# Performance work log

Hardware: AMD Instinct MI355X
Metric: run time of the kernel (lower is better)

The kernel has to match this reference:

```python
import jax, jax.numpy as jnp
import numpy as np

B, S, A, H, E = 8192, 256, 64, 1024, 8
IN = S + A
OUT = S + 1


def setup_inputs() -> dict:
    key = jax.random.key(0)
    ks = jax.random.split(key, 8)
    state = jax.random.normal(ks[0], (B, S), dtype=jnp.float32)
    action = jax.random.normal(ks[1], (B, A), dtype=jnp.float32)
    idx = jax.random.randint(ks[2], (B,), 0, E, dtype=jnp.int32)
    # Kaiming-ish scaling to keep activations sane
    W1 = jax.random.normal(ks[3], (E, IN, H), dtype=jnp.float32) / np.sqrt(IN)
    b1 = jnp.zeros((E, H), dtype=jnp.float32)
    W2 = jax.random.normal(ks[4], (E, H, H), dtype=jnp.float32) / np.sqrt(H)
    b2 = jnp.zeros((E, H), dtype=jnp.float32)
    W3 = jax.random.normal(ks[5], (E, H, OUT), dtype=jnp.float32) / np.sqrt(H)
    b3 = jnp.zeros((E, OUT), dtype=jnp.float32)
    return {"state": state, "action": action, "idx": idx,
            "W1": W1, "b1": b1, "W2": W2, "b2": b2, "W3": W3, "b3": b3}


def reference(state, action, idx, W1, b1, W2, b2, W3, b3):
    # Dense-MoE style: run all E experts on the full batch, then select the
    # per-sample expert output chosen by idx (matches masked gather/scatter
    # in the torch predict loop).
    x = jnp.concatenate([state, action], axis=-1)                  # [B, IN]
    h = jax.nn.relu(jnp.einsum('bi,eih->beh', x, W1) + b1)         # [B, E, H]
    h = jax.nn.relu(jnp.einsum('beh,ehk->bek', h, W2) + b2)        # [B, E, H]
    out = jnp.einsum('beh,eho->beo', h, W3) + b3                   # [B, E, S+1]
    sel = jnp.take_along_axis(out, idx[:, None, None], axis=1)[:, 0]  # [B, S+1]
    s_dim = state.shape[-1]
    delta = sel[:, :s_dim]
    reward = sel[:, s_dim:]
    next_state = state + delta
    return next_state, reward
```

## Files before the change

kernel.cpp:

```cpp
#include <hip/hip_runtime.h>
#include <stdint.h>

#define B_SZ   8192
#define IN_DIM 320
#define H_DIM  1024
#define E_NUM  8
#define OUT_DIM 257
#define TM     64
#define MAXT   (B_SZ / TM + E_NUM)

typedef __bf16 bf16x8 __attribute__((ext_vector_type(8)));
typedef float  f32x4  __attribute__((ext_vector_type(4)));

typedef unsigned int __attribute__((address_space(1))) as1_uint;
typedef unsigned int __attribute__((address_space(3))) as3_uint;

__device__ __forceinline__ void gload_lds16(const void* g, void* l) {
    __builtin_amdgcn_global_load_lds((const as1_uint*)g, (as3_uint*)l, 16, 0, 0);
}

__device__ __forceinline__ unsigned short f2bf(float f) {
    unsigned int u = __float_as_uint(f);
    return (unsigned short)((u + 0x7fffu + ((u >> 16) & 1u)) >> 16);
}

__global__ __launch_bounds__(256)
void k_prep(const float* __restrict__ state, const float* __restrict__ action,
            const int* __restrict__ idx,
            const float* __restrict__ W1, const float* __restrict__ W2,
            const float* __restrict__ W3,
            unsigned short* __restrict__ xb, unsigned short* __restrict__ w1t,
            unsigned short* __restrict__ w2t, unsigned short* __restrict__ w3t,
            int* __restrict__ order, int* __restrict__ te,
            int* __restrict__ tp0, int* __restrict__ tcnt) {
    __shared__ unsigned short tileU[64][65];
    __shared__ int scnt[16][E_NUM];
    int bid = blockIdx.x, tid = threadIdx.x;

    if (bid == 0) {
        int shard = tid & 15;
        if (tid < 128) ((int*)scnt)[tid] = 0;
        __syncthreads();
        for (int b = tid; b < B_SZ; b += 256) atomicAdd(&scnt[shard][idx[b]], 1);
        __syncthreads();
        if (tid == 0) {
            int pos = 0, tt = 0;
            for (int e = 0; e < E_NUM; e++) {
                int start = pos;
                for (int s = 0; s < 16; s++) { int c = scnt[s][e]; scnt[s][e] = pos; pos += c; }
                int tot = pos - start;
                for (int st = 0; st < tot; st += TM) {
                    te[tt] = e; tp0[tt] = start + st; tcnt[tt] = min(TM, tot - st); tt++;
                }
            }
            for (; tt < MAXT; tt++) { te[tt] = 0; tp0[tt] = 0; tcnt[tt] = 0; }
        }
        __syncthreads();
        for (int b = tid; b < B_SZ; b += 256) {
            int e = idx[b];
            int p = atomicAdd(&scnt[shard][e], 1);
            order[p] = b;
        }
        return;
    }

    if (bid <= 2560) {
        int q = (bid - 1) * 256 + tid;
        int b = q / 80, j = q % 80;
        float4 v = (j < 64) ? ((const float4*)state)[b * 64 + j]
                            : ((const float4*)action)[b * 16 + (j - 64)];
        ushort4 o;
        o.x = f2bf(v.x); o.y = f2bf(v.y); o.z = f2bf(v.z); o.w = f2bf(v.w);
        ((ushort4*)xb)[q] = o;
        return;
    }

    if (bid < 5761) {
        int e, kt, nt, K, Nsrc, dstRows; bool vec;
        const float* src; unsigned short* dst;
        if (bid < 3201) {
            int r = bid - 2561; e = r / 80; int m = r % 80; kt = m / 16; nt = m % 16;
            K = IN_DIM; Nsrc = H_DIM; dstRows = H_DIM; src = W1; dst = w1t; vec = true;
        } else if (bid < 5249) {
            int r = bid - 3201; e = r / 256; int m = r % 256; kt = m / 16; nt = m % 16;
            K = H_DIM; Nsrc = H_DIM; dstRows = H_DIM; src = W2; dst = w2t; vec = true;
        } else {
            int r = bid - 5249; e = r / 64; int m = r % 64; kt = m / 4; nt = m % 4;
            K = H_DIM; Nsrc = OUT_DIM; dstRows = 320; src = W3; dst = w3t; vec = false;
        }
        int k0 = kt * 64, n0 = nt * 64;
        const float* s = src + (size_t)e * K * Nsrc;
        unsigned short* d = dst + (size_t)e * dstRows * K;
        int c4 = (tid & 15) * 4;
        int rb = tid >> 4;

#pragma unroll
        for (int p = 0; p < 4; p++) {
            int r = rb + p * 16;
            const float* sp = s + (size_t)(k0 + r) * Nsrc + n0 + c4;
            float4 v;
            if (vec) v = *(const float4*)sp;
            else { v.x = sp[0]; v.y = sp[1]; v.z = sp[2]; v.w = sp[3]; }
            tileU[r][c4 + 0] = f2bf(v.x);
            tileU[r][c4 + 1] = f2bf(v.y);
            tileU[r][c4 + 2] = f2bf(v.z);
            tileU[r][c4 + 3] = f2bf(v.w);
        }
        __syncthreads();
#pragma unroll
        for (int p = 0; p < 4; p++) {
            int n = rb + p * 16;
            ushort4 o;
            o.x = tileU[c4 + 0][n];
            o.y = tileU[c4 + 1][n];
            o.z = tileU[c4 + 2][n];
            o.w = tileU[c4 + 3][n];
            *(ushort4*)&d[(size_t)(n0 + n) * K + k0 + c4] = o;
        }
        return;
    }

    int i = (bid - 5761) * 256 + tid;
    int e = i >> 10, k = i & 1023;
    w3t[((size_t)e * 320 + 256) * H_DIM + k] =
        f2bf(W3[((size_t)e * H_DIM + k) * OUT_DIM + 256]);
}

template <int K, int TN, int WN, bool GATHER, int MODE>
__global__ __launch_bounds__(256, 2)
void k_gemm(const unsigned short* __restrict__ Abase,
            const unsigned short* __restrict__ Wt, int wtRows,
            const float* __restrict__ bias, int bstride,
            unsigned short* __restrict__ Hout,
            float* __restrict__ Out, const float* __restrict__ state,
            const int* __restrict__ order,
            const int* __restrict__ te, const int* __restrict__ tp0,
            const int* __restrict__ tcnt) {
    constexpr int NI  = K / 32;
    constexpr int NF  = WN / 16;
    constexpr int ABY = 64 * 64;
    constexpr int BBY = TN * 64;
    constexpr int STG = ABY + BBY;
    __shared__ __align__(16) char lds[2 * STG];

    int t = blockIdx.x;
    int cnt = tcnt[t];
    if (cnt == 0) return;
    int e = te[t], p0 = tp0[t];
    int n0 = blockIdx.y * TN;
    int tid = threadIdx.x;
    int w = tid >> 6, lane = tid & 63;

    int r  = tid >> 2;
    int cg = (tid & 3) ^ ((r >> 1) & 3);
    int rc = r < cnt ? r : cnt - 1;
    long arow = GATHER ? order[p0 + rc] : (p0 + rc);
    const unsigned short* aP = Abase + (size_t)arow * K + cg * 8;
    const unsigned short* bP = Wt + ((size_t)e * wtRows + n0 + r) * K + cg * 8;

    auto stage = [&](int k0, int sb) {
        gload_lds16(aP + k0, lds + sb + tid * 16);
        gload_lds16(bP + k0, lds + sb + ABY + tid * 16);
        if (TN == 128)
            gload_lds16(bP + (size_t)64 * K + k0, lds + sb + ABY + 4096 + tid * 16);
    };

    f32x4 acc[4][NF];
#pragma unroll
    for (int i = 0; i < 4; i++)
#pragma unroll
        for (int j = 0; j < NF; j++) acc[i][j] = (f32x4)0.f;

    const int fm   = lane & 15;
    const int kc   = lane >> 4;
    const int koff = ((kc ^ ((fm >> 1) & 3)) * 8);

    stage(0, 0);
    for (int it = 0; it < NI; ++it) {
        __syncthreads();
        if (it + 1 < NI) stage((it + 1) * 32, ((it + 1) & 1) * STG);
        const unsigned short* As = (const unsigned short*)(lds + (it & 1) * STG);
        const unsigned short* Bs = As + ABY / 2;

        bf16x8 af[4], bf[NF];
#pragma unroll
        for (int i = 0; i < 4; i++)
            af[i] = *(const bf16x8*)&As[(i * 16 + fm) * 32 + koff];
#pragma unroll
        for (int j = 0; j < NF; j++)
            bf[j] = *(const bf16x8*)&Bs[(w * WN + j * 16 + fm) * 32 + koff];
#pragma unroll
        for (int i = 0; i < 4; i++)
#pragma unroll
            for (int j = 0; j < NF; j++)
                acc[i][j] = __builtin_amdgcn_mfma_f32_16x16x32_bf16(
                    af[i], bf[j], acc[i][j], 0, 0, 0);
    }

    int col = lane & 15, rq = lane >> 4;
#pragma unroll
    for (int j = 0; j < NF; j++) {
        int n = n0 + w * WN + j * 16 + col;
        float bv = (MODE == 0) ? bias[e * bstride + n]
                               : ((n <= 256) ? bias[e * bstride + n] : 0.f);
#pragma unroll
        for (int i = 0; i < 4; i++) {
#pragma unroll
            for (int rr = 0; rr < 4; rr++) {
                int m = i * 16 + rq * 4 + rr;
                if (m < cnt) {
                    float v = acc[i][j][rr] + bv;
                    if (MODE == 0) {
                        Hout[(size_t)(p0 + m) * H_DIM + n] = f2bf(fmaxf(v, 0.f));
                    } else {
                        int row = order[p0 + m];
                        if (n < 256) {
                            size_t o = (size_t)row * 256 + n;
                            Out[o] = state[o] + v;
                        } else if (n == 256) {
                            Out[(size_t)B_SZ * 256 + row] = v;
                        }
                    }
                }
            }
        }
    }
}

extern "C" void kernel_launch(void* const* d_in, const int* in_sizes, int n_in,
                              void* d_out, int out_size, void* d_ws, size_t ws_size,
                              hipStream_t stream) {
    const float* state  = (const float*)d_in[0];
    const float* action = (const float*)d_in[1];
    const int*   idx    = (const int*)d_in[2];
    const float* W1     = (const float*)d_in[3];
    const float* b1     = (const float*)d_in[4];
    const float* W2     = (const float*)d_in[5];
    const float* b2     = (const float*)d_in[6];
    const float* W3     = (const float*)d_in[7];
    const float* b3     = (const float*)d_in[8];
    float* out = (float*)d_out;

    char* ws = (char*)d_ws;
    size_t off = 0;
    auto alloc = [&](size_t bytes) -> void* {
        void* p = ws + off;
        off = (off + bytes + 255) & ~(size_t)255;
        return p;
    };
    unsigned short* xb  = (unsigned short*)alloc((size_t)B_SZ * IN_DIM * 2);
    unsigned short* w1t = (unsigned short*)alloc((size_t)E_NUM * H_DIM * IN_DIM * 2);
    unsigned short* w2t = (unsigned short*)alloc((size_t)E_NUM * H_DIM * H_DIM * 2);
    unsigned short* w3t = (unsigned short*)alloc((size_t)E_NUM * 320 * H_DIM * 2);
    unsigned short* h1  = (unsigned short*)alloc((size_t)B_SZ * H_DIM * 2);
    unsigned short* h2  = (unsigned short*)alloc((size_t)B_SZ * H_DIM * 2);
    int* order = (int*)alloc(B_SZ * 4);
    int* te    = (int*)alloc(MAXT * 4);
    int* tp0   = (int*)alloc(MAXT * 4);
    int* tcnt  = (int*)alloc(MAXT * 4);

    k_prep<<<5793, 256, 0, stream>>>(state, action, idx, W1, W2, W3,
                                     xb, w1t, w2t, w3t, order, te, tp0, tcnt);

    k_gemm<IN_DIM, 128, 32, true, 0><<<dim3(MAXT, 8), 256, 0, stream>>>(
        xb, w1t, H_DIM, b1, H_DIM, h1, nullptr, nullptr, order, te, tp0, tcnt);
    k_gemm<H_DIM, 128, 32, false, 0><<<dim3(MAXT, 8), 256, 0, stream>>>(
        h1, w2t, H_DIM, b2, H_DIM, h2, nullptr, nullptr, order, te, tp0, tcnt);
    k_gemm<H_DIM, 64, 16, false, 1><<<dim3(MAXT, 5), 256, 0, stream>>>(
        h2, w3t, 320, b3, OUT_DIM, nullptr, out, state, order, te, tp0, tcnt);
}
```

Baseline: 225.7 us.

## Enlarge grouped GEMM M-tile to 128 rows with 2x2 wave layout

Doubles the per-block row tile from 64 to 128 tokens and arranges the four waves as a 2x2 grid (two along M, two along N) instead of four waves along N. Each weight tile loaded into LDS is now reused across twice as many rows, which cuts weight traffic and halves the number of row tiles. The cost is more LDS per block, fewer blocks in flight, and more padding waste in the last partial tile of each expert.

Measured after the change: 227.6 us. No clear change (+0.9%).

```diff
diff --git a/kernel.cpp b/kernel.cpp
--- a/kernel.cpp
+++ b/kernel.cpp
@@ -6,7 +6,7 @@
 #define H_DIM  1024
 #define E_NUM  8
 #define OUT_DIM 257
-#define TM     64
+#define TM     128
 #define MAXT   (B_SZ / TM + E_NUM)
 
 typedef __bf16 bf16x8 __attribute__((ext_vector_type(8)));
@@ -126,7 +126,7 @@
         f2bf(W3[((size_t)e * H_DIM + k) * OUT_DIM + 256]);
 }
 
-template <int K, int TN, int WN, bool GATHER, int MODE>
+template <int K, int TN, bool GATHER, int MODE>
 __global__ __launch_bounds__(256, 2)
 void k_gemm(const unsigned short* __restrict__ Abase,
             const unsigned short* __restrict__ Wt, int wtRows,
@@ -137,10 +137,12 @@
             const int* __restrict__ te, const int* __restrict__ tp0,
             const int* __restrict__ tcnt) {
     constexpr int NI  = K / 32;
+    constexpr int WN  = TN / 2;
     constexpr int NF  = WN / 16;
-    constexpr int ABY = 64 * 64;
+    constexpr int ABY = 128 * 64;
     constexpr int BBY = TN * 64;
     constexpr int STG = ABY + BBY;
+    constexpr int BL  = TN / 64;
     __shared__ __align__(16) char lds[2 * STG];
 
     int t = blockIdx.x;
@@ -150,19 +152,25 @@
     int n0 = blockIdx.y * TN;
     int tid = threadIdx.x;
     int w = tid >> 6, lane = tid & 63;
-
-    int r  = tid >> 2;
-    int cg = (tid & 3) ^ ((r >> 1) & 3);
-    int rc = r < cnt ? r : cnt - 1;
-    long arow = GATHER ? order[p0 + rc] : (p0 + rc);
-    const unsigned short* aP = Abase + (size_t)arow * K + cg * 8;
-    const unsigned short* bP = Wt + ((size_t)e * wtRows + n0 + r) * K + cg * 8;
+    int wm = w >> 1, wn = w & 1;
+
+    int r0 = tid >> 2;
+    int cg = (tid & 3) ^ ((r0 >> 1) & 3);
+    int rc0 = r0 < cnt ? r0 : cnt - 1;
+    int rc1 = (r0 + 64) < cnt ? (r0 + 64) : cnt - 1;
+    long a0 = GATHER ? order[p0 + rc0] : (p0 + rc0);
+    long a1 = GATHER ? order[p0 + rc1] : (p0 + rc1);
+    const unsigned short* aP0 = Abase + (size_t)a0 * K + cg * 8;
+    const unsigned short* aP1 = Abase + (size_t)a1 * K + cg * 8;
+    const unsigned short* bP0 = Wt + ((size_t)e * wtRows + n0 + r0) * K + cg * 8;
+    const unsigned short* bP1 = bP0 + (size_t)64 * K;
 
     auto stage = [&](int k0, int sb) {
-        gload_lds16(aP + k0, lds + sb + tid * 16);
-        gload_lds16(bP + k0, lds + sb + ABY + tid * 16);
-        if (TN == 128)
-            gload_lds16(bP + (size_t)64 * K + k0, lds + sb + ABY + 4096 + tid * 16);
+        gload_lds16(aP0 + k0, lds + sb + tid * 16);
+        gload_lds16(aP1 + k0, lds + sb + 4096 + tid * 16);
+        gload_lds16(bP0 + k0, lds + sb + ABY + tid * 16);
+        if (BL == 2)
+            gload_lds16(bP1 + k0, lds + sb + ABY + 4096 + tid * 16);
     };
 
     f32x4 acc[4][NF];
@@ -179,8 +187,9 @@
     for (int it = 0; it < NI; ++it) {
         __syncthreads();
         if (it + 1 < NI) stage((it + 1) * 32, ((it + 1) & 1) * STG);
-        const unsigned short* As = (const unsigned short*)(lds + (it & 1) * STG);
-        const unsigned short* Bs = As + ABY / 2;
+        const unsigned short* Ls = (const unsigned short*)(lds + (it & 1) * STG);
+        const unsigned short* As = Ls + wm * 64 * 32;
+        const unsigned short* Bs = Ls + ABY / 2 + wn * WN * 32;
 
         bf16x8 af[4], bf[NF];
 #pragma unroll
@@ -188,7 +197,7 @@
             af[i] = *(const bf16x8*)&As[(i * 16 + fm) * 32 + koff];
 #pragma unroll
         for (int j = 0; j < NF; j++)
-            bf[j] = *(const bf16x8*)&Bs[(w * WN + j * 16 + fm) * 32 + koff];
+            bf[j] = *(const bf16x8*)&Bs[(j * 16 + fm) * 32 + koff];
 #pragma unroll
         for (int i = 0; i < 4; i++)
 #pragma unroll
@@ -200,14 +209,14 @@
     int col = lane & 15, rq = lane >> 4;
 #pragma unroll
     for (int j = 0; j < NF; j++) {
-        int n = n0 + w * WN + j * 16 + col;
+        int n = n0 + wn * WN + j * 16 + col;
         float bv = (MODE == 0) ? bias[e * bstride + n]
                                : ((n <= 256) ? bias[e * bstride + n] : 0.f);
 #pragma unroll
         for (int i = 0; i < 4; i++) {
 #pragma unroll
             for (int rr = 0; rr < 4; rr++) {
-                int m = i * 16 + rq * 4 + rr;
+                int m = wm * 64 + i * 16 + rq * 4 + rr;
                 if (m < cnt) {
                     float v = acc[i][j][rr] + bv;
                     if (MODE == 0) {
@@ -262,10 +271,10 @@
     k_prep<<<5793, 256, 0, stream>>>(state, action, idx, W1, W2, W3,
                                      xb, w1t, w2t, w3t, order, te, tp0, tcnt);
 
-    k_gemm<IN_DIM, 128, 32, true, 0><<<dim3(MAXT, 8), 256, 0, stream>>>(
+    k_gemm<IN_DIM, 128, true, 0><<<dim3(MAXT, 8), 256, 0, stream>>>(
         xb, w1t, H_DIM, b1, H_DIM, h1, nullptr, nullptr, order, te, tp0, tcnt);
-    k_gemm<H_DIM, 128, 32, false, 0><<<dim3(MAXT, 8), 256, 0, stream>>>(
+    k_gemm<H_DIM, 128, false, 0><<<dim3(MAXT, 8), 256, 0, stream>>>(
         h1, w2t, H_DIM, b2, H_DIM, h2, nullptr, nullptr, order, te, tp0, tcnt);
-    k_gemm<H_DIM, 64, 16, false, 1><<<dim3(MAXT, 5), 256, 0, stream>>>(
+    k_gemm<H_DIM, 64, false, 1><<<dim3(MAXT, 5), 256, 0, stream>>>(
         h2, w3t, 320, b3, OUT_DIM, nullptr, out, state, order, te, tp0, tcnt);
 }
```

## Use 128x128 tiles with a K=64 stage, 2x2 warp layout, and coarser prep blocks

Applied to the files above, without the earlier changes.

Restructures the grouped GEMM so each stage loads a 64-wide K slice with an 8-chunk XOR swizzle. Warps are arranged 2x2 over the output tile, and layers 1-2 switch to 128x128 tiles with their own 128-row tile schedule and a swapped grid order, so blocks sharing an expert tile run close together. The aim is more MFMA work per LDS load and fewer sync points per unit of work. The prep kernel is also coarsened so each block handles several tiles, cutting the block count. Larger tiles mean more padding waste on partial expert groups and fewer blocks to fill the CUs.

Result: slower. 235.1 us (+4.2%).

```diff
diff --git a/kernel.cpp b/kernel.cpp
--- a/kernel.cpp
+++ b/kernel.cpp
@@ -6,8 +6,8 @@
 #define H_DIM  1024
 #define E_NUM  8
 #define OUT_DIM 257
-#define TM     64
-#define MAXT   (B_SZ / TM + E_NUM)
+#define MAXT1  72
+#define MAXT2  136
 
 typedef __bf16 bf16x8 __attribute__((ext_vector_type(8)));
 typedef float  f32x4  __attribute__((ext_vector_type(4)));
@@ -31,8 +31,9 @@
             const float* __restrict__ W3,
             unsigned short* __restrict__ xb, unsigned short* __restrict__ w1t,
             unsigned short* __restrict__ w2t, unsigned short* __restrict__ w3t,
-            int* __restrict__ order, int* __restrict__ te,
-            int* __restrict__ tp0, int* __restrict__ tcnt) {
+            int* __restrict__ order,
+            int* __restrict__ te1, int* __restrict__ tp1, int* __restrict__ tc1,
+            int* __restrict__ te2, int* __restrict__ tp2, int* __restrict__ tc2) {
     __shared__ unsigned short tileU[64][65];
     __shared__ int scnt[16][E_NUM];
     int bid = blockIdx.x, tid = threadIdx.x;
@@ -44,16 +45,20 @@
         for (int b = tid; b < B_SZ; b += 256) atomicAdd(&scnt[shard][idx[b]], 1);
         __syncthreads();
         if (tid == 0) {
-            int pos = 0, tt = 0;
+            int pos = 0, t1 = 0, t2 = 0;
             for (int e = 0; e < E_NUM; e++) {
                 int start = pos;
                 for (int s = 0; s < 16; s++) { int c = scnt[s][e]; scnt[s][e] = pos; pos += c; }
                 int tot = pos - start;
-                for (int st = 0; st < tot; st += TM) {
-                    te[tt] = e; tp0[tt] = start + st; tcnt[tt] = min(TM, tot - st); tt++;
+                for (int st = 0; st < tot; st += 128) {
+                    te1[t1] = e; tp1[t1] = start + st; tc1[t1] = min(128, tot - st); t1++;
                 }
-            }
-            for (; tt < MAXT; tt++) { te[tt] = 0; tp0[tt] = 0; tcnt[tt] = 0; }
+                for (int st = 0; st < tot; st += 64) {
+                    te2[t2] = e; tp2[t2] = start + st; tc2[t2] = min(64, tot - st); t2++;
+                }
+            }
+            for (; t1 < MAXT1; t1++) { te1[t1] = 0; tp1[t1] = 0; tc1[t1] = 0; }
+            for (; t2 < MAXT2; t2++) { te2[t2] = 0; tp2[t2] = 0; tc2[t2] = 0; }
         }
         __syncthreads();
         for (int b = tid; b < B_SZ; b += 256) {
@@ -64,69 +69,78 @@
         return;
     }
 
-    if (bid <= 2560) {
-        int q = (bid - 1) * 256 + tid;
-        int b = q / 80, j = q % 80;
-        float4 v = (j < 64) ? ((const float4*)state)[b * 64 + j]
-                            : ((const float4*)action)[b * 16 + (j - 64)];
-        ushort4 o;
-        o.x = f2bf(v.x); o.y = f2bf(v.y); o.z = f2bf(v.z); o.w = f2bf(v.w);
-        ((ushort4*)xb)[q] = o;
+    if (bid <= 320) {
+#pragma unroll
+        for (int k = 0; k < 8; k++) {
+            int q = ((bid - 1) * 8 + k) * 256 + tid;
+            int b = q / 80, j = q % 80;
+            float4 v = (j < 64) ? ((const float4*)state)[b * 64 + j]
+                                : ((const float4*)action)[b * 16 + (j - 64)];
+            ushort4 o;
+            o.x = f2bf(v.x); o.y = f2bf(v.y); o.z = f2bf(v.z); o.w = f2bf(v.w);
+            ((ushort4*)xb)[q] = o;
+        }
         return;
     }
 
-    if (bid < 5761) {
-        int e, kt, nt, K, Nsrc, dstRows; bool vec;
+    if (bid <= 992) {
+        int e, nt, kt0, nkt, K, Nsrc, dstRows; bool vec;
         const float* src; unsigned short* dst;
-        if (bid < 3201) {
-            int r = bid - 2561; e = r / 80; int m = r % 80; kt = m / 16; nt = m % 16;
+        if (bid <= 448) {
+            int b = bid - 321; e = b >> 4; nt = b & 15;
+            kt0 = 0; nkt = 5;
             K = IN_DIM; Nsrc = H_DIM; dstRows = H_DIM; src = W1; dst = w1t; vec = true;
-        } else if (bid < 5249) {
-            int r = bid - 3201; e = r / 256; int m = r % 256; kt = m / 16; nt = m % 16;
+        } else if (bid <= 960) {
+            int b = bid - 449; e = b >> 6; int r = b & 63;
+            nt = r >> 2; kt0 = (r & 3) * 4; nkt = 4;
             K = H_DIM; Nsrc = H_DIM; dstRows = H_DIM; src = W2; dst = w2t; vec = true;
         } else {
-            int r = bid - 5249; e = r / 64; int m = r % 64; kt = m / 4; nt = m % 4;
+            int b = bid - 961; e = b >> 2; nt = b & 3;
+            kt0 = 0; nkt = 16;
             K = H_DIM; Nsrc = OUT_DIM; dstRows = 320; src = W3; dst = w3t; vec = false;
         }
-        int k0 = kt * 64, n0 = nt * 64;
         const float* s = src + (size_t)e * K * Nsrc;
         unsigned short* d = dst + (size_t)e * dstRows * K;
         int c4 = (tid & 15) * 4;
         int rb = tid >> 4;
-
-#pragma unroll
-        for (int p = 0; p < 4; p++) {
-            int r = rb + p * 16;
-            const float* sp = s + (size_t)(k0 + r) * Nsrc + n0 + c4;
-            float4 v;
-            if (vec) v = *(const float4*)sp;
-            else { v.x = sp[0]; v.y = sp[1]; v.z = sp[2]; v.w = sp[3]; }
-            tileU[r][c4 + 0] = f2bf(v.x);
-            tileU[r][c4 + 1] = f2bf(v.y);
-            tileU[r][c4 + 2] = f2bf(v.z);
-            tileU[r][c4 + 3] = f2bf(v.w);
-        }
-        __syncthreads();
-#pragma unroll
-        for (int p = 0; p < 4; p++) {
-            int n = rb + p * 16;
-            ushort4 o;
-            o.x = tileU[c4 + 0][n];
-            o.y = tileU[c4 + 1][n];
-            o.z = tileU[c4 + 2][n];
-            o.w = tileU[c4 + 3][n];
-            *(ushort4*)&d[(size_t)(n0 + n) * K + k0 + c4] = o;
+        int n0 = nt * 64;
+        for (int kt = kt0; kt < kt0 + nkt; kt++) {
+            int k0 = kt * 64;
+#pragma unroll
+            for (int p = 0; p < 4; p++) {
+                int r = rb + p * 16;
+                const float* sp = s + (size_t)(k0 + r) * Nsrc + n0 + c4;
+                float4 v;
+                if (vec) v = *(const float4*)sp;
+                else { v.x = sp[0]; v.y = sp[1]; v.z = sp[2]; v.w = sp[3]; }
+                tileU[r][c4 + 0] = f2bf(v.x);
+                tileU[r][c4 + 1] = f2bf(v.y);
+                tileU[r][c4 + 2] = f2bf(v.z);
+                tileU[r][c4 + 3] = f2bf(v.w);
+            }
+            __syncthreads();
+#pragma unroll
+            for (int p = 0; p < 4; p++) {
+                int n = rb + p * 16;
+                ushort4 o;
+                o.x = tileU[c4 + 0][n];
+                o.y = tileU[c4 + 1][n];
+                o.z = tileU[c4 + 2][n];
+                o.w = tileU[c4 + 3][n];
+                *(ushort4*)&d[(size_t)(n0 + n) * K + k0 + c4] = o;
+            }
+            __syncthreads();
         }
         return;
     }
 
-    int i = (bid - 5761) * 256 + tid;
+    int i = (bid - 993) * 256 + tid;
     int e = i >> 10, k = i & 1023;
     w3t[((size_t)e * 320 + 256) * H_DIM + k] =
         f2bf(W3[((size_t)e * H_DIM + k) * OUT_DIM + 256]);
 }
 
-template <int K, int TN, int WN, bool GATHER, int MODE>
+template <int K, int TM, int TN, bool GATHER, int MODE, bool SWAPXY>
 __global__ __launch_bounds__(256, 2)
 void k_gemm(const unsigned short* __restrict__ Abase,
             const unsigned short* __restrict__ Wt, int wtRows,
@@ -136,78 +150,103 @@
             const int* __restrict__ order,
             const int* __restrict__ te, const int* __restrict__ tp0,
             const int* __restrict__ tcnt) {
-    constexpr int NI  = K / 32;
-    constexpr int NF  = WN / 16;
-    constexpr int ABY = 64 * 64;
-    constexpr int BBY = TN * 64;
+    constexpr int NI  = K / 64;
+    constexpr int WM  = TM / 2, MF = WM / 16;
+    constexpr int WN  = TN / 2, NF = WN / 16;
+    constexpr int ABY = TM * 128;
+    constexpr int BBY = TN * 128;
     constexpr int STG = ABY + BBY;
+    constexpr int AL  = TM / 32;
+    constexpr int BL  = TN / 32;
     __shared__ __align__(16) char lds[2 * STG];
 
-    int t = blockIdx.x;
+    int t  = SWAPXY ? blockIdx.y : blockIdx.x;
+    int ny = SWAPXY ? blockIdx.x : blockIdx.y;
     int cnt = tcnt[t];
     if (cnt == 0) return;
     int e = te[t], p0 = tp0[t];
-    int n0 = blockIdx.y * TN;
+    int n0 = ny * TN;
     int tid = threadIdx.x;
     int w = tid >> 6, lane = tid & 63;
-
-    int r  = tid >> 2;
-    int cg = (tid & 3) ^ ((r >> 1) & 3);
-    int rc = r < cnt ? r : cnt - 1;
-    long arow = GATHER ? order[p0 + rc] : (p0 + rc);
-    const unsigned short* aP = Abase + (size_t)arow * K + cg * 8;
-    const unsigned short* bP = Wt + ((size_t)e * wtRows + n0 + r) * K + cg * 8;
-
-    auto stage = [&](int k0, int sb) {
-        gload_lds16(aP + k0, lds + sb + tid * 16);
-        gload_lds16(bP + k0, lds + sb + ABY + tid * 16);
-        if (TN == 128)
-            gload_lds16(bP + (size_t)64 * K + k0, lds + sb + ABY + 4096 + tid * 16);
+    int wm = w >> 1, wn = w & 1;
+
+    int r0 = tid >> 3;
+    int c  = tid & 7;
+    int cg2 = c ^ (r0 & 7);
+    const unsigned short* aP[AL];
+#pragma unroll
+    for (int k = 0; k < AL; k++) {
+        int r = r0 + 32 * k;
+        int rc = r < cnt ? r : cnt - 1;
+        long ar = GATHER ? order[p0 + rc] : (p0 + rc);
+        aP[k] = Abase + (size_t)ar * K + cg2 * 8;
+    }
+    const unsigned short* bP[BL];
+#pragma unroll
+    for (int k = 0; k < BL; k++)
+        bP[k] = Wt + ((size_t)e * wtRows + n0 + r0 + 32 * k) * K + cg2 * 8;
+
+    auto stage = [&](int k0s, int sb) {
+#pragma unroll
+        for (int k = 0; k < AL; k++)
+            gload_lds16(aP[k] + k0s, lds + sb + tid * 16 + k * 4096);
+#pragma unroll
+        for (int k = 0; k < BL; k++)
+            gload_lds16(bP[k] + k0s, lds + sb + ABY + tid * 16 + k * 4096);
     };
 
-    f32x4 acc[4][NF];
-#pragma unroll
-    for (int i = 0; i < 4; i++)
+    f32x4 acc[MF][NF];
+#pragma unroll
+    for (int i = 0; i < MF; i++)
 #pragma unroll
         for (int j = 0; j < NF; j++) acc[i][j] = (f32x4)0.f;
 
-    const int fm   = lane & 15;
-    const int kc   = lane >> 4;
-    const int koff = ((kc ^ ((fm >> 1) & 3)) * 8);
+    const int fm = lane & 15;
+    const int kc = lane >> 4;
 
     stage(0, 0);
     for (int it = 0; it < NI; ++it) {
         __syncthreads();
-        if (it + 1 < NI) stage((it + 1) * 32, ((it + 1) & 1) * STG);
-        const unsigned short* As = (const unsigned short*)(lds + (it & 1) * STG);
-        const unsigned short* Bs = As + ABY / 2;
-
-        bf16x8 af[4], bf[NF];
-#pragma unroll
-        for (int i = 0; i < 4; i++)
-            af[i] = *(const bf16x8*)&As[(i * 16 + fm) * 32 + koff];
-#pragma unroll
-        for (int j = 0; j < NF; j++)
-            bf[j] = *(const bf16x8*)&Bs[(w * WN + j * 16 + fm) * 32 + koff];
-#pragma unroll
-        for (int i = 0; i < 4; i++)
-#pragma unroll
-            for (int j = 0; j < NF; j++)
-                acc[i][j] = __builtin_amdgcn_mfma_f32_16x16x32_bf16(
-                    af[i], bf[j], acc[i][j], 0, 0, 0);
+        if (it + 1 < NI) stage((it + 1) * 64, ((it + 1) & 1) * STG);
+        const unsigned short* Ls = (const unsigned short*)(lds + (it & 1) * STG);
+        const unsigned short* As = Ls + wm * WM * 64;
+        const unsigned short* Bs = Ls + ABY / 2 + wn * WN * 64;
+
+#pragma unroll
+        for (int ko = 0; ko < 2; ko++) {
+            bf16x8 af[MF], bf[NF];
+#pragma unroll
+            for (int i = 0; i < MF; i++) {
+                int ri = i * 16 + fm;
+                int ce = (4 * ko + kc) ^ (ri & 7);
+                af[i] = *(const bf16x8*)&As[ri * 64 + ce * 8];
+            }
+#pragma unroll
+            for (int j = 0; j < NF; j++) {
+                int rj = j * 16 + fm;
+                int ce = (4 * ko + kc) ^ (rj & 7);
+                bf[j] = *(const bf16x8*)&Bs[rj * 64 + ce * 8];
+            }
+#pragma unroll
+            for (int i = 0; i < MF; i++)
+#pragma unroll
+                for (int j = 0; j < NF; j++)
+                    acc[i][j] = __builtin_amdgcn_mfma_f32_16x16x32_bf16(
+                        af[i], bf[j], acc[i][j], 0, 0, 0);
+        }
     }
 
     int col = lane & 15, rq = lane >> 4;
 #pragma unroll
     for (int j = 0; j < NF; j++) {
-        int n = n0 + w * WN + j * 16 + col;
+        int n = n0 + wn * WN + j * 16 + col;
         float bv = (MODE == 0) ? bias[e * bstride + n]
                                : ((n <= 256) ? bias[e * bstride + n] : 0.f);
 #pragma unroll
-        for (int i = 0; i < 4; i++) {
+        for (int i = 0; i < MF; i++) {
 #pragma unroll
             for (int rr = 0; rr < 4; rr++) {
-                int m = i * 16 + rq * 4 + rr;
+                int m = wm * WM + i * 16 + rq * 4 + rr;
                 if (m < cnt) {
                     float v = acc[i][j][rr] + bv;
                     if (MODE == 0) {
@@ -255,17 +294,21 @@
     unsigned short* h1  = (unsigned short*)alloc((size_t)B_SZ * H_DIM * 2);
     unsigned short* h2  = (unsigned short*)alloc((size_t)B_SZ * H_DIM * 2);
     int* order = (int*)alloc(B_SZ * 4);
-    int* te    = (int*)alloc(MAXT * 4);
-    int* tp0   = (int*)alloc(MAXT * 4);
-    int* tcnt  = (int*)alloc(MAXT * 4);
-
-    k_prep<<<5793, 256, 0, stream>>>(state, action, idx, W1, W2, W3,
-                                     xb, w1t, w2t, w3t, order, te, tp0, tcnt);
-
-    k_gemm<IN_DIM, 128, 32, true, 0><<<dim3(MAXT, 8), 256, 0, stream>>>(
-        xb, w1t, H_DIM, b1, H_DIM, h1, nullptr, nullptr, order, te, tp0, tcnt);
-    k_gemm<H_DIM, 128, 32, false, 0><<<dim3(MAXT, 8), 256, 0, stream>>>(
-        h1, w2t, H_DIM, b2, H_DIM, h2, nullptr, nullptr, order, te, tp0, tcnt);
-    k_gemm<H_DIM, 64, 16, false, 1><<<dim3(MAXT, 5), 256, 0, stream>>>(
-        h2, w3t, 320, b3, OUT_DIM, nullptr, out, state, order, te, tp0, tcnt);
-}
+    int* te1   = (int*)alloc(MAXT1 * 4);
+    int* tp1   = (int*)alloc(MAXT1 * 4);
+    int* tc1   = (int*)alloc(MAXT1 * 4);
+    int* te2   = (int*)alloc(MAXT2 * 4);
+    int* tp2   = (int*)alloc(MAXT2 * 4);
+    int* tc2   = (int*)alloc(MAXT2 * 4);
+
+    k_prep<<<1025, 256, 0, stream>>>(state, action, idx, W1, W2, W3,
+                                     xb, w1t, w2t, w3t, order,
+                                     te1, tp1, tc1, te2, tp2, tc2);
+
+    k_gemm<IN_DIM, 128, 128, true, 0, true><<<dim3(8, MAXT1), 256, 0, stream>>>(
+        xb, w1t, H_DIM, b1, H_DIM, h1, nullptr, nullptr, order, te1, tp1, tc1);
+    k_gemm<H_DIM, 128, 128, false, 0, true><<<dim3(8, MAXT1), 256, 0, stream>>>(
+        h1, w2t, H_DIM, b2, H_DIM, h2, nullptr, nullptr, order, te1, tp1, tc1);
+    k_gemm<H_DIM, 64, 64, false, 1, false><<<dim3(MAXT2, 5), 256, 0, stream>>>(
+        h2, w3t, 320, b3, OUT_DIM, nullptr, out, state, order, te2, tp2, tc2);
+}
```
